# Performance work log

Hardware: AMD Instinct MI355X
Metric: run time of the kernel (lower is better)

## Reference

```python
import jax, jax.numpy as jnp
import numpy as np

N_NODES = 50000
NEG_SLOPE = 0.2  # PyG GATConv default


def setup_inputs() -> dict:
    key = jax.random.key(0)
    ks = jax.random.split(key, 10)
    N, D_IN, HID, H, D_OUT, E = N_NODES, 256, 64, 4, 40, 800000
    inp = {
        "x": jax.random.normal(ks[0], (N, D_IN), jnp.float32),
        "edge_index": jax.random.randint(ks[1], (2, E), 0, N, jnp.int32),
        "W1": jax.random.normal(ks[2], (D_IN, H * HID), jnp.float32) * (1.0 / np.sqrt(D_IN)),
        "att_src1": jax.random.normal(ks[3], (H, HID), jnp.float32) * 0.1,
        "att_dst1": jax.random.normal(ks[4], (H, HID), jnp.float32) * 0.1,
        "b1": jnp.zeros((H * HID,), jnp.float32),
        "W2": jax.random.normal(ks[5], (H * HID, D_OUT), jnp.float32) * (1.0 / np.sqrt(H * HID)),
        "att_src2": jax.random.normal(ks[6], (1, D_OUT), jnp.float32) * 0.1,
        "att_dst2": jax.random.normal(ks[7], (1, D_OUT), jnp.float32) * 0.1,
        "b2": jnp.zeros((D_OUT,), jnp.float32),
    }
    return inp


def _gat_conv(x, src, dst, W, a_src, a_dst, b, n_nodes):
    """One GATConv layer (PyG semantics, self-loops already in src/dst)."""
    H, F = a_src.shape
    h = (x @ W).reshape(n_nodes, H, F)                      # [N,H,F]
    a_s = jnp.einsum('nhf,hf->nh', h, a_src)                # [N,H]
    a_d = jnp.einsum('nhf,hf->nh', h, a_dst)                # [N,H]
    e = jax.nn.leaky_relu(a_s[src] + a_d[dst], NEG_SLOPE)   # [E,H]
    # segment softmax over incoming edges of each destination node
    m = jax.ops.segment_max(e, dst, num_segments=n_nodes)   # [N,H]
    ex = jnp.exp(e - m[dst])                                # [E,H]
    den = jax.ops.segment_sum(ex, dst, num_segments=n_nodes)
    alpha = ex / den[dst]                                   # [E,H]
    out = jax.ops.segment_sum(h[src] * alpha[:, :, None], dst, num_segments=n_nodes)
    return out.reshape(n_nodes, H * F) + b


def reference(x, edge_index, W1, att_src1, att_dst1, b1, W2, att_src2, att_dst2, b2):
    N = x.shape[0]
    loop = jnp.arange(N, dtype=edge_index.dtype)
    src = jnp.concatenate([edge_index[0], loop])
    dst = jnp.concatenate([edge_index[1], loop])
    h = jax.nn.relu(_gat_conv(x, src, dst, W1, att_src1, att_dst1, b1, N))
    logits = _gat_conv(h, src, dst, W2, att_src2, att_dst2, b2, N)
    return jax.nn.log_softmax(logits, axis=1)
```

## Files before the change

### kernel.cpp

```cpp
#include <hip/hip_runtime.h>
#include <hip/hip_fp16.h>
#include <math.h>

#define NEG_SLOPE 0.2f

typedef short short8v __attribute__((ext_vector_type(8)));
typedef _Float16 half8v __attribute__((ext_vector_type(8)));
typedef float f32x4 __attribute__((ext_vector_type(4)));

__device__ __forceinline__ unsigned short f2bf(float f) {
    unsigned int u = __builtin_bit_cast(unsigned int, f);
    u += 0x7FFFu + ((u >> 16) & 1u);
    return (unsigned short)(u >> 16);
}

__device__ __forceinline__ void fma_h4(float4& acc, float w, uint2 v) {
    __half2 p0 = __builtin_bit_cast(__half2, v.x);
    __half2 p1 = __builtin_bit_cast(__half2, v.y);
    float2 f0 = __half22float2(p0), f1 = __half22float2(p1);
    acc.x += w * f0.x; acc.y += w * f0.y; acc.z += w * f1.x; acc.w += w * f1.y;
}

__global__ void k_deg(const int* __restrict__ ei, int E, int N, int* __restrict__ deg, int* __restrict__ rank) {
    int i = blockIdx.x * blockDim.x + threadIdx.x;
    int Et = E + N;
    if (i >= Et) return;
    int dst = (i < E) ? ei[E + i] : (i - E);
    rank[i] = atomicAdd(&deg[dst], 1);
}

__global__ void k_scan_block(const int* __restrict__ deg, int N, int* __restrict__ excl, int* __restrict__ bsums) {
    __shared__ int s[256];
    int b = blockIdx.x, t = threadIdx.x;
    int i = b * 256 + t;
    int v = (i < N) ? deg[i] : 0;
    s[t] = v;
    __syncthreads();
    for (int off = 1; off < 256; off <<= 1) {
        int add = (t >= off) ? s[t - off] : 0;
        __syncthreads();
        s[t] += add;
        __syncthreads();
    }
    int incl = s[t];
    if (i < N) excl[i] = incl - v;
    if (t == 255) bsums[b] = incl;
}

__global__ void k_scan_sums(int* __restrict__ bsums, int NB) {
    __shared__ int s[256];
    int t = threadIdx.x;
    int v = (t < NB) ? bsums[t] : 0;
    s[t] = v;
    __syncthreads();
    for (int off = 1; off < 256; off <<= 1) {
        int add = (t >= off) ? s[t - off] : 0;
        __syncthreads();
        s[t] += add;
        __syncthreads();
    }
    if (t < NB) bsums[t] = s[t] - v;
}

__global__ void k_scan_add(int* __restrict__ row_start, const int* __restrict__ bsums, int N, int Et) {
    int i = blockIdx.x * blockDim.x + threadIdx.x;
    if (i < N) row_start[i] += bsums[blockIdx.x];
    if (i == 0) row_start[N] = Et;
}

__global__ void k_scatter(const int* __restrict__ ei, const int* __restrict__ rank, int E, int N,
                          const int* __restrict__ row_start, int* __restrict__ csr_src) {
    int i = blockIdx.x * blockDim.x + threadIdx.x;
    int Et = E + N;
    if (i >= Et) return;
    int src, dst;
    if (i < E) { src = ei[i]; dst = ei[E + i]; }
    else       { src = i - E; dst = i - E; }
    csr_src[row_start[dst] + rank[i]] = src;
}

__global__ void k_cvt_w(const float* __restrict__ W1, const float* __restrict__ W2,
                        unsigned short* __restrict__ w1t, __half* __restrict__ w2t) {
    int b = blockIdx.x, k = threadIdx.x;
    if (b < 256) {
        w1t[b * 256 + k] = f2bf(W1[k * 256 + b]);
    } else {
        int c = b - 256;
        w2t[c * 256 + k] = __float2half((c < 40) ? W2[k * 40 + c] : 0.f);
    }
}

#define LDP 264
__global__ __launch_bounds__(256) void k_gemm1_mfma(const float* __restrict__ x,
                                                    const unsigned short* __restrict__ w1t,
                                                    const float* __restrict__ att_s,
                                                    const float* __restrict__ att_d,
                                                    __half* __restrict__ h1h,
                                                    float* __restrict__ as1, float* __restrict__ ad1, int N) {
    __shared__ unsigned short As[64 * LDP];
    __shared__ unsigned short Bs[64 * LDP];
    int tid = threadIdx.x;
    int row0 = blockIdx.x * 64;
#pragma unroll
    for (int it = 0; it < 16; it++) {
        int c = tid + it * 256;
        int r = c >> 6, q = c & 63;
        float4 v = make_float4(0, 0, 0, 0);
        if (row0 + r < N) v = ((const float4*)x)[(size_t)(row0 + r) * 64 + q];
        ushort4 o;
        o.x = f2bf(v.x); o.y = f2bf(v.y); o.z = f2bf(v.z); o.w = f2bf(v.w);
        *(ushort4*)&As[r * LDP + q * 4] = o;
    }
    int w = tid >> 6, l = tid & 63;
    int hi = l >> 4, lo = l & 15;
    for (int head = 0; head < 4; head++) {
#pragma unroll
        for (int it = 0; it < 8; it++) {
            int c = tid + it * 256;
            int r = c >> 5, q = c & 31;
            uint4 vb = ((const uint4*)w1t)[(size_t)(head * 64 + r) * 32 + q];
            *(uint4*)&Bs[r * LDP + q * 8] = vb;
        }
        __syncthreads();
        f32x4 acc[4] = {};
#pragma unroll
        for (int kk = 0; kk < 8; kk++) {
            short8v a = *(const short8v*)&As[(16 * w + lo) * LDP + kk * 32 + 8 * hi];
#pragma unroll
            for (int jb = 0; jb < 4; jb++) {
                short8v b = *(const short8v*)&Bs[(16 * jb + lo) * LDP + kk * 32 + 8 * hi];
                acc[jb] = __builtin_amdgcn_mfma_f32_16x16x32_bf16(a, b, acc[jb], 0, 0, 0);
            }
        }
        float asr[4], adr[4];
#pragma unroll
        for (int jb = 0; jb < 4; jb++) {
            int c = head * 64 + lo + 16 * jb;
            asr[jb] = att_s[c];
            adr[jb] = att_d[c];
        }
#pragma unroll
        for (int j = 0; j < 4; j++) {
            int rr = 16 * w + 4 * hi + j;
            int r = row0 + rr;
            float s = 0.f, d = 0.f;
#pragma unroll
            for (int jb = 0; jb < 4; jb++) {
                float v = acc[jb][j];
                s += v * asr[jb];
                d += v * adr[jb];
                if (r < N) h1h[(size_t)r * 256 + head * 64 + lo + 16 * jb] = __float2half(v);
            }
            s += __shfl_xor(s, 1); s += __shfl_xor(s, 2); s += __shfl_xor(s, 4); s += __shfl_xor(s, 8);
            d += __shfl_xor(d, 1); d += __shfl_xor(d, 2); d += __shfl_xor(d, 4); d += __shfl_xor(d, 8);
            if (lo == 0 && r < N) {
                as1[r * 4 + head] = s;
                ad1[r * 4 + head] = d;
            }
        }
        if (head < 3) __syncthreads();
    }
}

__global__ __launch_bounds__(256) void k_agg1(const __half* __restrict__ h1h, const float* __restrict__ as1,
                                              const float* __restrict__ ad1, const int* __restrict__ row_start,
                                              const int* __restrict__ csr_src, const float* __restrict__ b1,
                                              __half* __restrict__ hbh, int N) {
    __shared__ int    s_src[4][64];
    __shared__ float4 s_w[4][64];
    int wv = threadIdx.x >> 6, l = threadIdx.x & 63;
    int n = blockIdx.x * 4 + wv;
    if (n >= N) return;
    int s0 = row_start[n], s1 = row_start[n + 1];
    int head = l >> 4;
    unsigned lb8 = (unsigned)l * 8u;
    const char* h1b = (const char*)h1h;
    float4 adv = ((const float4*)ad1)[n];
    float4 acc0 = make_float4(0, 0, 0, 0), acc1 = acc0, acc2 = acc0, acc3 = acc0;
    float den = 0.f;
    for (int c0 = s0; c0 < s1; c0 += 64) {
        int cl = min(64, s1 - c0);
        if (l < cl) {
            int si = csr_src[c0 + l];
            s_src[wv][l] = si;
            float4 a = ((const float4*)as1)[si];
            float4 e;
            e.x = a.x + adv.x; e.x = e.x > 0.f ? e.x : NEG_SLOPE * e.x; e.x = __expf(e.x);
            e.y = a.y + adv.y; e.y = e.y > 0.f ? e.y : NEG_SLOPE * e.y; e.y = __expf(e.y);
            e.z = a.z + adv.z; e.z = e.z > 0.f ? e.z : NEG_SLOPE * e.z; e.z = __expf(e.z);
            e.w = a.w + adv.w; e.w = e.w > 0.f ? e.w : NEG_SLOPE * e.w; e.w = __expf(e.w);
            s_w[wv][l] = e;
        }
        int p = 0;
        for (; p + 4 <= cl; p += 4) {
            int sA = s_src[wv][p],     sB = s_src[wv][p + 1];
            int sC = s_src[wv][p + 2], sD = s_src[wv][p + 3];
            float wA = ((const float*)&s_w[wv][p    ])[head];
            float wB = ((const float*)&s_w[wv][p + 1])[head];
            float wC = ((const float*)&s_w[wv][p + 2])[head];
            float wD = ((const float*)&s_w[wv][p + 3])[head];
            uint2 vA = *(const uint2*)(h1b + (unsigned)sA * 512u + lb8);
            uint2 vB = *(const uint2*)(h1b + (unsigned)sB * 512u + lb8);
            uint2 vC = *(const uint2*)(h1b + (unsigned)sC * 512u + lb8);
            uint2 vD = *(const uint2*)(h1b + (unsigned)sD * 512u + lb8);
            den += (wA + wB) + (wC + wD);
            fma_h4(acc0, wA, vA); fma_h4(acc1, wB, vB);
            fma_h4(acc2, wC, vC); fma_h4(acc3, wD, vD);
        }
        for (; p < cl; p++) {
            int s = s_src[wv][p];
            float wg = ((const float*)&s_w[wv][p])[head];
            uint2 v = *(const uint2*)(h1b + (unsigned)s * 512u + lb8);
            den += wg;
            fma_h4(acc0, wg, v);
        }
    }
    float4 acc;
    acc.x = (acc0.x + acc1.x) + (acc2.x + acc3.x);
    acc.y = (acc0.y + acc1.y) + (acc2.y + acc3.y);
    acc.z = (acc0.z + acc1.z) + (acc2.z + acc3.z);
    acc.w = (acc0.w + acc1.w) + (acc2.w + acc3.w);
    float inv = 1.f / den;
    float4 b = ((const float4*)b1)[l];
    float r0 = acc.x * inv + b.x; r0 = r0 > 0.f ? r0 : 0.f;
    float r1 = acc.y * inv + b.y; r1 = r1 > 0.f ? r1 : 0.f;
    float r2 = acc.z * inv + b.z; r2 = r2 > 0.f ? r2 : 0.f;
    float r3 = acc.w * inv + b.w; r3 = r3 > 0.f ? r3 : 0.f;
    unsigned short u0 = __builtin_bit_cast(unsigned short, __float2half(r0));
    unsigned short u1 = __builtin_bit_cast(unsigned short, __float2half(r1));
    unsigned short u2 = __builtin_bit_cast(unsigned short, __float2half(r2));
    unsigned short u3 = __builtin_bit_cast(unsigned short, __float2half(r3));
    uint2 st;
    st.x = (unsigned)u0 | ((unsigned)u1 << 16);
    st.y = (unsigned)u2 | ((unsigned)u3 << 16);
    *(uint2*)((char*)hbh + (unsigned)n * 512u + lb8) = st;
}

__global__ __launch_bounds__(256) void k_gemm2_mfma(const _Float16* __restrict__ hbh,
                                                    const _Float16* __restrict__ w2t,
                                                    const float* __restrict__ att_s2,
                                                    const float* __restrict__ att_d2,
                                                    __half* __restrict__ h2h,
                                                    float* __restrict__ as2, float* __restrict__ ad2, int N) {
    int tid = threadIdx.x, w = tid >> 6, l = tid & 63;
    int hi = l >> 4, lo = l & 15;
    int row0 = blockIdx.x * 64;
    int arow = row0 + 16 * w + lo;
    const char* hb = (const char*)hbh;
    f32x4 acc[3] = {};
#pragma unroll
    for (int kk = 0; kk < 8; kk++) {
        half8v a = {};
        if (arow < N) a = *(const half8v*)(hb + (unsigned)arow * 512u + (unsigned)(kk * 64 + 16 * hi));
#pragma unroll
        for (int jb = 0; jb < 3; jb++) {
            half8v b = *(const half8v*)&w2t[(16 * jb + lo) * 256 + kk * 32 + 8 * hi];
            acc[jb] = __builtin_amdgcn_mfma_f32_16x16x32_f16(a, b, acc[jb], 0, 0, 0);
        }
    }
    float asr[3], adr[3];
#pragma unroll
    for (int jb = 0; jb < 3; jb++) {
        int c = 16 * jb + lo;
        asr[jb] = (c < 40) ? att_s2[c] : 0.f;
        adr[jb] = (c < 40) ? att_d2[c] : 0.f;
    }
#pragma unroll
    for (int j = 0; j < 4; j++) {
        int r = row0 + 16 * w + 4 * hi + j;
        float s = 0.f, d = 0.f;
#pragma unroll
        for (int jb = 0; jb < 3; jb++) {
            float v = acc[jb][j];
            s += v * asr[jb];
            d += v * adr[jb];
            int c = 16 * jb + lo;
            if (c < 40 && r < N) h2h[(size_t)r * 40 + c] = __float2half(v);
        }
        s += __shfl_xor(s, 1); s += __shfl_xor(s, 2); s += __shfl_xor(s, 4); s += __shfl_xor(s, 8);
        d += __shfl_xor(d, 1); d += __shfl_xor(d, 2); d += __shfl_xor(d, 4); d += __shfl_xor(d, 8);
        if (lo == 0 && r < N) { as2[r] = s; ad2[r] = d; }
    }
}

__global__ __launch_bounds__(256) void k_agg2(const __half* __restrict__ h2h, const float* __restrict__ as2,
                                              const float* __restrict__ ad2, const int* __restrict__ row_start,
                                              const int* __restrict__ csr_src, const float* __restrict__ b2,
                                              float* __restrict__ out, int N) {
    __shared__ int   s_src[4][64];
    __shared__ float s_w[4][64];
    int wv = threadIdx.x >> 6, l = threadIdx.x & 63;
    int n = blockIdx.x * 4 + wv;
    if (n >= N) return;
    int s0 = row_start[n], s1 = row_start[n + 1];
    int grp = l / 20, li = l - grp * 20;
    unsigned li4 = (unsigned)li * 4u;
    const char* h2b = (const char*)h2h;
    float ad = ad2[n];
    float2 acc = make_float2(0.f, 0.f);
    float den = 0.f;
    bool act = grp < 3;
    for (int c0 = s0; c0 < s1; c0 += 64) {
        int cl = min(64, s1 - c0);
        if (l < cl) {
            int si = csr_src[c0 + l];
            s_src[wv][l] = si;
            float e = as2[si] + ad;
            e = e > 0.f ? e : NEG_SLOPE * e;
            s_w[wv][l] = __expf(e);
        }
        if (act) {
            for (int p = grp; p < cl; p += 3) {
                int si = s_src[wv][p];
                float w = s_w[wv][p];
                unsigned v = *(const unsigned*)(h2b + (unsigned)si * 80u + li4);
                den += w;
                float2 f = __half22float2(__builtin_bit_cast(__half2, v));
                acc.x += w * f.x; acc.y += w * f.y;
            }
        }
    }
    float den_t = __shfl(den, li) + __shfl(den, 20 + li) + __shfl(den, 40 + li);
    float ax = acc.x + __shfl(acc.x, l + 20) + __shfl(acc.x, l + 40);
    float ay = acc.y + __shfl(acc.y, l + 20) + __shfl(acc.y, l + 40);
    float inv = 1.f / den_t;
    float lg0 = -1e30f, lg1 = -1e30f;
    if (l < 20) {
        lg0 = ax * inv + b2[2 * l];
        lg1 = ay * inv + b2[2 * l + 1];
    }
    float mx = fmaxf(lg0, lg1);
    for (int off = 32; off; off >>= 1) mx = fmaxf(mx, __shfl_xor(mx, off));
    float s = (l < 20) ? (__expf(lg0 - mx) + __expf(lg1 - mx)) : 0.f;
    for (int off = 32; off; off >>= 1) s += __shfl_xor(s, off);
    float ls = logf(s);
    if (l < 20) {
        out[(size_t)n * 40 + 2 * l]     = lg0 - mx - ls;
        out[(size_t)n * 40 + 2 * l + 1] = lg1 - mx - ls;
    }
}

extern "C" void kernel_launch(void* const* d_in, const int* in_sizes, int n_in,
                              void* d_out, int out_size, void* d_ws, size_t ws_size,
                              hipStream_t stream) {
    const float* x      = (const float*)d_in[0];
    const int*   ei     = (const int*)d_in[1];
    const float* W1     = (const float*)d_in[2];
    const float* att_s1 = (const float*)d_in[3];
    const float* att_d1 = (const float*)d_in[4];
    const float* b1     = (const float*)d_in[5];
    const float* W2     = (const float*)d_in[6];
    const float* att_s2 = (const float*)d_in[7];
    const float* att_d2 = (const float*)d_in[8];
    const float* b2     = (const float*)d_in[9];

    int N = in_sizes[0] / 256;
    int E = in_sizes[1] / 2;
    int Et = E + N;

    char* ws = (char*)d_ws;
    size_t off = 0;
    auto alloc = [&](size_t bytes) -> void* {
        void* p = ws + off;
        off += (bytes + 255) / 256 * 256;
        return p;
    };
    __half* h1h = (__half*)alloc((size_t)N * 256 * 2);
    __half* hbh = (__half*)alloc((size_t)N * 256 * 2);
    __half* h2h = (__half*)alloc((size_t)N * 40 * 2);
    unsigned short* w1t = (unsigned short*)alloc((size_t)256 * 256 * 2);
    __half* w2t = (__half*)alloc((size_t)48 * 256 * 2);
    float* as1 = (float*)alloc((size_t)N * 4 * 4);
    float* ad1 = (float*)alloc((size_t)N * 4 * 4);
    float* as2 = (float*)alloc((size_t)N * 4);
    float* ad2 = (float*)alloc((size_t)N * 4);
    int* deg       = (int*)alloc((size_t)N * 4);
    int* rank      = (int*)alloc((size_t)Et * 4);
    int* row_start = (int*)alloc((size_t)(N + 1) * 4);
    int* csr_src   = (int*)alloc((size_t)Et * 4);
    int NB = (N + 255) / 256;
    int* bsums = (int*)alloc((size_t)NB * 4);

    hipMemsetAsync(deg, 0, (size_t)N * 4, stream);

    k_deg<<<(Et + 255) / 256, 256, 0, stream>>>(ei, E, N, deg, rank);
    k_scan_block<<<NB, 256, 0, stream>>>(deg, N, row_start, bsums);
    k_scan_sums<<<1, 256, 0, stream>>>(bsums, NB);
    k_scan_add<<<NB, 256, 0, stream>>>(row_start, bsums, N, Et);
    k_scatter<<<(Et + 255) / 256, 256, 0, stream>>>(ei, rank, E, N, row_start, csr_src);

    k_cvt_w<<<304, 256, 0, stream>>>(W1, W2, w1t, w2t);

    k_gemm1_mfma<<<(N + 63) / 64, 256, 0, stream>>>(x, w1t, att_s1, att_d1, h1h, as1, ad1, N);
    k_agg1<<<(N + 3) / 4, 256, 0, stream>>>(h1h, as1, ad1, row_start, csr_src, b1, hbh, N);
    k_gemm2_mfma<<<(N + 63) / 64, 256, 0, stream>>>((const _Float16*)hbh, (const _Float16*)w2t,
                                                    att_s2, att_d2, h2h, as2, ad2, N);
    k_agg2<<<(N + 3) / 4, 256, 0, stream>>>(h2h, as2, ad2, row_start, csr_src, b2, (float*)d_out, N);
}
```

Before: 217.1 us.

## Load GEMM1 B operand from global, hoist A fragments, unroll aggregation gathers

The layer-1 GEMM no longer stages W1 tiles in shared memory. Each wave keeps its A fragments in registers and reads B fragments directly from the small, L2-resident transposed weight, which drops the per-head barriers and half the LDS footprint. The layer-1 aggregation gets an 8-way unrolled gather so more independent loads are in flight. Layer-2 aggregation splits its accumulators in two to expose more memory-level parallelism. The risk is uncoalesced global B reads in the GEMM and higher register pressure in the unrolled loops.

```diff
diff --git a/kernel.cpp b/kernel.cpp
--- a/kernel.cpp
+++ b/kernel.cpp
@@ -98,7 +98,6 @@
                                                     __half* __restrict__ h1h,
                                                     float* __restrict__ as1, float* __restrict__ ad1, int N) {
     __shared__ unsigned short As[64 * LDP];
-    __shared__ unsigned short Bs[64 * LDP];
     int tid = threadIdx.x;
     int row0 = blockIdx.x * 64;
 #pragma unroll
@@ -111,25 +110,22 @@
         o.x = f2bf(v.x); o.y = f2bf(v.y); o.z = f2bf(v.z); o.w = f2bf(v.w);
         *(ushort4*)&As[r * LDP + q * 4] = o;
     }
+    __syncthreads();
     int w = tid >> 6, l = tid & 63;
     int hi = l >> 4, lo = l & 15;
+    short8v a[8];
+#pragma unroll
+    for (int kk = 0; kk < 8; kk++)
+        a[kk] = *(const short8v*)&As[(16 * w + lo) * LDP + kk * 32 + 8 * hi];
     for (int head = 0; head < 4; head++) {
-#pragma unroll
-        for (int it = 0; it < 8; it++) {
-            int c = tid + it * 256;
-            int r = c >> 5, q = c & 31;
-            uint4 vb = ((const uint4*)w1t)[(size_t)(head * 64 + r) * 32 + q];
-            *(uint4*)&Bs[r * LDP + q * 8] = vb;
-        }
-        __syncthreads();
         f32x4 acc[4] = {};
 #pragma unroll
         for (int kk = 0; kk < 8; kk++) {
-            short8v a = *(const short8v*)&As[(16 * w + lo) * LDP + kk * 32 + 8 * hi];
 #pragma unroll
             for (int jb = 0; jb < 4; jb++) {
-                short8v b = *(const short8v*)&Bs[(16 * jb + lo) * LDP + kk * 32 + 8 * hi];
-                acc[jb] = __builtin_amdgcn_mfma_f32_16x16x32_bf16(a, b, acc[jb], 0, 0, 0);
+                short8v b = *(const short8v*)&w1t[(unsigned)(head * 64 + 16 * jb + lo) * 256u
+                                                  + (unsigned)(kk * 32 + 8 * hi)];
+                acc[jb] = __builtin_amdgcn_mfma_f32_16x16x32_bf16(a[kk], b, acc[jb], 0, 0, 0);
             }
         }
         float asr[4], adr[4];
@@ -158,7 +154,6 @@
                 ad1[r * 4 + head] = d;
             }
         }
-        if (head < 3) __syncthreads();
     }
 }
 
@@ -192,6 +187,25 @@
             s_w[wv][l] = e;
         }
         int p = 0;
+        for (; p + 8 <= cl; p += 8) {
+            int ss[8]; float ww[8]; uint2 vv[8];
+#pragma unroll
+            for (int i = 0; i < 8; i++) {
+                ss[i] = s_src[wv][p + i];
+                ww[i] = ((const float*)&s_w[wv][p + i])[head];
+            }
+#pragma unroll
+            for (int i = 0; i < 8; i++)
+                vv[i] = *(const uint2*)(h1b + (unsigned)ss[i] * 512u + lb8);
+#pragma unroll
+            for (int i = 0; i < 8; i++) {
+                den += ww[i];
+                if ((i & 3) == 0) fma_h4(acc0, ww[i], vv[i]);
+                if ((i & 3) == 1) fma_h4(acc1, ww[i], vv[i]);
+                if ((i & 3) == 2) fma_h4(acc2, ww[i], vv[i]);
+                if ((i & 3) == 3) fma_h4(acc3, ww[i], vv[i]);
+            }
+        }
         for (; p + 4 <= cl; p += 4) {
             int sA = s_src[wv][p],     sB = s_src[wv][p + 1];
             int sC = s_src[wv][p + 2], sD = s_src[wv][p + 3];
@@ -297,8 +311,8 @@
     unsigned li4 = (unsigned)li * 4u;
     const char* h2b = (const char*)h2h;
     float ad = ad2[n];
-    float2 acc = make_float2(0.f, 0.f);
-    float den = 0.f;
+    float2 accA = make_float2(0.f, 0.f), accB = accA;
+    float denA = 0.f, denB = 0.f;
     bool act = grp < 3;
     for (int c0 = s0; c0 < s1; c0 += 64) {
         int cl = min(64, s1 - c0);
@@ -310,16 +324,30 @@
             s_w[wv][l] = __expf(e);
         }
         if (act) {
-            for (int p = grp; p < cl; p += 3) {
+            int p = grp;
+            for (; p + 3 < cl; p += 6) {
+                int sA = s_src[wv][p], sB = s_src[wv][p + 3];
+                float wA = s_w[wv][p], wB = s_w[wv][p + 3];
+                unsigned vA = *(const unsigned*)(h2b + (unsigned)sA * 80u + li4);
+                unsigned vB = *(const unsigned*)(h2b + (unsigned)sB * 80u + li4);
+                denA += wA; denB += wB;
+                float2 fA = __half22float2(__builtin_bit_cast(__half2, vA));
+                float2 fB = __half22float2(__builtin_bit_cast(__half2, vB));
+                accA.x += wA * fA.x; accA.y += wA * fA.y;
+                accB.x += wB * fB.x; accB.y += wB * fB.y;
+            }
+            for (; p < cl; p += 3) {
                 int si = s_src[wv][p];
                 float w = s_w[wv][p];
                 unsigned v = *(const unsigned*)(h2b + (unsigned)si * 80u + li4);
-                den += w;
+                denA += w;
                 float2 f = __half22float2(__builtin_bit_cast(__half2, v));
-                acc.x += w * f.x; acc.y += w * f.y;
-            }
-        }
-    }
+                accA.x += w * f.x; accA.y += w * f.y;
+            }
+        }
+    }
+    float den = denA + denB;
+    float2 acc = make_float2(accA.x + accB.x, accA.y + accB.y);
     float den_t = __shfl(den, li) + __shfl(den, 20 + li) + __shfl(den, 40 + li);
     float ax = acc.x + __shfl(acc.x, l + 20) + __shfl(acc.x, l + 40);
     float ay = acc.y + __shfl(acc.y, l + 20) + __shfl(acc.y, l + 40);
```

After: 252.6 us. 1.16x slower.
